# Performance work log

Measured on AMD Instinct MI355X. Metric: run time of the kernel, lower is better.

## Reference

```python
import jax, jax.numpy as jnp
import numpy as np

R_CUT = 5.0
N_NODES = 50000
N_EDGES = 400000
N_GRAPHS = 2500
D = 128        # embedding_size (hardcoded by torch.split(..., 128))
N_RBF = 20
N_BLOCKS = 3
PI = 3.141592653589793


def setup_inputs() -> dict:
    key = jax.random.key(0)
    ks = jax.random.split(key, 32)
    w = lambda k, s: (jax.random.normal(k, s) * 0.05).astype(jnp.float32)
    z = jax.random.randint(ks[0], (N_NODES,), 0, 100)
    edges = jax.random.randint(ks[1], (N_EDGES, 2), 0, N_NODES)
    r_ij = jax.random.uniform(ks[2], (N_EDGES, 1), minval=0.8, maxval=R_CUT, dtype=jnp.float32)
    d = jax.random.normal(ks[3], (N_EDGES, 3), dtype=jnp.float32)
    r_ij_normalized = d / jnp.linalg.norm(d, axis=1, keepdims=True)
    graph_idx = jax.random.randint(ks[4], (N_NODES,), 0, N_GRAPHS)
    return {
        "z": z, "edges": edges, "r_ij": r_ij,
        "r_ij_normalized": r_ij_normalized, "graph_idx": graph_idx,
        "emb": w(ks[5], (100, D)),
        # message blocks (stacked over N_BLOCKS)
        "msg_w1": w(ks[6], (N_BLOCKS, D, D)),   "msg_b1": w(ks[7], (N_BLOCKS, D)),
        "msg_w2": w(ks[8], (N_BLOCKS, D, 3 * D)), "msg_b2": w(ks[9], (N_BLOCKS, 3 * D)),
        "rbf_w": w(ks[10], (N_BLOCKS, N_RBF, 3 * D)), "rbf_b": w(ks[11], (N_BLOCKS, 3 * D)),
        # update blocks
        "upd_U": w(ks[12], (N_BLOCKS, D, D)), "upd_V": w(ks[13], (N_BLOCKS, D, D)),
        "upd_w1": w(ks[14], (N_BLOCKS, 2 * D, D)), "upd_b1": w(ks[15], (N_BLOCKS, D)),
        "upd_w2": w(ks[16], (N_BLOCKS, D, 3 * D)), "upd_b2": w(ks[17], (N_BLOCKS, 3 * D)),
        # readout
        "blue_w1": w(ks[18], (D, D)), "blue_b1": w(ks[19], (D,)),
        "blue_w2": w(ks[20], (D, 1)), "blue_b2": w(ks[21], (1,)),
    }


def _rbf(r, r_cut):
    n = jnp.arange(1, N_RBF + 1, dtype=r.dtype)  # [20]
    return jnp.sin(n * PI / r_cut * r) / r        # [E,20]


def _fcut(r, r_cut):
    return jnp.where(r <= r_cut, 0.5 * (jnp.cos(PI * r / r_cut) + 1.0), 0.0)


def painn_forward(z, edges, r_ij, r_ij_normalized, graph_idx, emb,
                  msg_w1, msg_b1, msg_w2, msg_b2, rbf_w, rbf_b,
                  upd_U, upd_V, upd_w1, upd_b1, upd_w2, upd_b2,
                  blue_w1, blue_b1, blue_w2, blue_b2):
    silu = jax.nn.silu
    src = edges[:, 1]  # gathered (neighbor j)
    dst = edges[:, 0]  # scattered (center i)
    s = emb[z]                                           # [N,128]
    v = jnp.zeros((s.shape[0], 3, D), dtype=r_ij.dtype)  # [N,3,128]
    rbf = _rbf(r_ij, R_CUT)                              # [E,20]
    f_c = _fcut(r_ij, R_CUT)                             # [E,1]
    for i in range(N_BLOCKS):
        # --- message block ---
        rbf_fcut = (rbf @ rbf_w[i] + rbf_b[i]) * f_c            # [E,384]
        s_pass = silu(s @ msg_w1[i] + msg_b1[i]) @ msg_w2[i] + msg_b2[i]  # [N,384]
        pass_out = rbf_fcut * s_pass[src]                        # [E,384]
        d_v, d_s, d_rep = jnp.split(pass_out, 3, axis=-1)        # each [E,128]
        delta_v = v[src] * d_v[:, None, :] + r_ij_normalized[:, :, None] * d_rep[:, None, :]
        s = s + jax.ops.segment_sum(d_s, dst, num_segments=N_NODES)
        v = v + jax.ops.segment_sum(delta_v, dst, num_segments=N_NODES)
        # --- update block ---
        U_v = jnp.einsum('nde,ef->ndf', v, upd_U[i])             # [N,3,128]
        V_v = jnp.einsum('nde,ef->ndf', v, upd_V[i])
        V_norm = jnp.linalg.norm(V_v, axis=1)                    # [N,128]
        sv = jnp.concatenate([V_norm, s], axis=1)                # [N,256]
        a = silu(sv @ upd_w1[i] + upd_b1[i]) @ upd_w2[i] + upd_b2[i]  # [N,384]
        avv, asv, ass = jnp.split(a, 3, axis=1)
        s = s + jnp.sum(U_v * V_v, axis=1) * asv + ass
        v = v + avv[:, None, :] * U_v
    blue = silu(s @ blue_w1 + blue_b1) @ blue_w2 + blue_b2       # [N,1]
    return jax.ops.segment_sum(blue, graph_idx, num_segments=N_GRAPHS)  # [G,1]


def reference(z, edges, r_ij, r_ij_normalized, graph_idx, emb,
              msg_w1, msg_b1, msg_w2, msg_b2, rbf_w, rbf_b,
              upd_U, upd_V, upd_w1, upd_b1, upd_w2, upd_b2,
              blue_w1, blue_b1, blue_w2, blue_b2):
    return painn_forward(z, edges, r_ij, r_ij_normalized, graph_idx, emb,
                         msg_w1, msg_b1, msg_w2, msg_b2, rbf_w, rbf_b,
                         upd_U, upd_V, upd_w1, upd_b1, upd_w2, upd_b2,
                         blue_w1, blue_b1, blue_w2, blue_b2)
```

## Files before the change

kernel.cpp:

```cpp
#include <hip/hip_runtime.h>
#include <hip/hip_bf16.h>
#include <math.h>

#define N_NODES 50000
#define N_EDGES 400000
#define N_GRAPHS 2500
#define D 128
#define D3 384
#define N_RBF 20
#define R_CUT 5.0f
#define PI_F 3.14159265358979f
#define NCH 98
#define GEB 16
#define GLDS_STRIDE 388

typedef __attribute__((ext_vector_type(8))) short bf16x8;
typedef __attribute__((ext_vector_type(4))) float f32x4;

__device__ __forceinline__ float silu_f(float x) {
    return x / (1.0f + __expf(-x));
}
__device__ __forceinline__ short f2bf(float x) {
    union { float f; unsigned u; } v; v.f = x;
    unsigned r = (v.u + 0x7FFFu + ((v.u >> 16) & 1u)) >> 16;
    return (short)r;
}
__device__ __forceinline__ float bf2f(short x) {
    union { unsigned u; float f; } v; v.u = ((unsigned)(unsigned short)x) << 16;
    return v.f;
}

#define MAXJOBS 19
struct PackJobs {
    const float* W[MAXJOBS];
    short* P[MAXJOBS];
    int K[MAXJOBS];
    int N[MAXJOBS];
    int boff[MAXJOBS + 1];
    int njobs;
};
__global__ void k_packall(PackJobs jobs) {
    int b = blockIdx.x;
    int j = 0;
    while (j + 1 < jobs.njobs && b >= jobs.boff[j + 1]) ++j;
    int t = (b - jobs.boff[j]) * 256 + threadIdx.x;
    int K = jobs.K[j], N = jobs.N[j];
    int NKT = K / 32;
    int total = (N / 16) * NKT * 64;
    if (t >= total) return;
    const float* W = jobs.W[j];
    short* P = jobs.P[j];
    int lane = t & 63;
    int kt = (t >> 6) % NKT;
    int nt = (t >> 6) / NKT;
    int k0 = kt * 32 + (lane >> 4) * 8;
    int col = nt * 16 + (lane & 15);
    #pragma unroll
    for (int q = 0; q < 8; ++q)
        P[(size_t)t * 8 + q] = f2bf(W[(size_t)(k0 + q) * N + col]);
}

__global__ void k_packrbf(const float* __restrict__ rbf_w, const float* __restrict__ rbf_b,
                          short* __restrict__ P) {
    int t = blockIdx.x * 256 + threadIdx.x;
    if (t >= 3 * 1536) return;
    int i = t / 1536;
    int r = t - i * 1536;
    int lane = r & 63;
    int nt = r >> 6;
    int col = nt * 16 + (lane & 15);
    int k0 = (lane >> 4) * 8;
    const float* W = rbf_w + (size_t)i * N_RBF * D3;
    const float* B = rbf_b + (size_t)i * D3;
    short* out = P + (size_t)i * 12288 + (size_t)r * 8;
    #pragma unroll
    for (int q = 0; q < 8; ++q) {
        int k = k0 + q;
        float v = (k < N_RBF) ? W[(size_t)k * D3 + col] : ((k == N_RBF) ? B[col] : 0.0f);
        out[q] = f2bf(v);
    }
}

template<int K, int N, bool SILU, int AMODE>
__global__ __launch_bounds__(256) void k_gemm(const void* __restrict__ Aptr,
                                              const void* __restrict__ A2ptr,
                                              const short* __restrict__ Bp,
                                              const float* __restrict__ bias,
                                              short* __restrict__ Cbf, int M) {
    constexpr int NKT = K / 32, NNT = N / 16;
    int lane = threadIdx.x & 63, wv = threadIdx.x >> 6;
    int tile = blockIdx.x * 4 + wv;
    int base = tile * 32;
    if (base >= M) return;
    bool has2 = (base + 16 < M);
    int r16 = lane & 15;
    int kgrp = (lane >> 4) * 8;
    int arow0 = base + r16;
    int arow1 = has2 ? (base + 16 + r16) : arow0;

    bf16x8 a0[NKT], a1[NKT];
    #pragma unroll
    for (int ss = 0; ss < 2; ++ss) {
        int arow = ss ? arow1 : arow0;
        bf16x8* a = ss ? a1 : a0;
        if (AMODE == 0) {
            const short* A = (const short*)Aptr + (size_t)arow * K + kgrp;
            #pragma unroll
            for (int kt = 0; kt < NKT; ++kt) a[kt] = *(const bf16x8*)(A + kt * 32);
        } else if (AMODE == 1) {
            const float* A = (const float*)Aptr + (size_t)arow * K + kgrp;
            #pragma unroll
            for (int kt = 0; kt < NKT; ++kt)
                #pragma unroll
                for (int j = 0; j < 8; ++j) a[kt][j] = f2bf(A[kt * 32 + j]);
        } else {
            const short* A1 = (const short*)Aptr + (size_t)arow * 128 + kgrp;
            const float* A2 = (const float*)A2ptr + (size_t)arow * 128 + kgrp;
            #pragma unroll
            for (int kt = 0; kt < 4 && kt < NKT; ++kt) a[kt] = *(const bf16x8*)(A1 + kt * 32);
            #pragma unroll
            for (int kt = 4; kt < NKT; ++kt)
                #pragma unroll
                for (int j = 0; j < 8; ++j) a[kt][j] = f2bf(A2[(kt - 4) * 32 + j]);
        }
    }

    int crow0 = base + (lane >> 4) * 4;
    int ccol = lane & 15;
    const bf16x8* Bv = (const bf16x8*)Bp;
    #pragma unroll
    for (int nt = 0; nt < NNT; ++nt) {
        f32x4 acc0 = {0.f, 0.f, 0.f, 0.f};
        f32x4 acc1 = {0.f, 0.f, 0.f, 0.f};
        #pragma unroll
        for (int kt = 0; kt < NKT; ++kt) {
            bf16x8 b = Bv[(nt * NKT + kt) * 64 + lane];
            acc0 = __builtin_amdgcn_mfma_f32_16x16x32_bf16(a0[kt], b, acc0, 0, 0, 0);
            acc1 = __builtin_amdgcn_mfma_f32_16x16x32_bf16(a1[kt], b, acc1, 0, 0, 0);
        }
        int col = nt * 16 + ccol;
        float bs = bias ? bias[col] : 0.0f;
        #pragma unroll
        for (int j = 0; j < 4; ++j) {
            float v = acc0[j] + bs;
            if (SILU) v = silu_f(v);
            Cbf[(size_t)(crow0 + j) * N + col] = f2bf(v);
        }
        if (has2) {
            #pragma unroll
            for (int j = 0; j < 4; ++j) {
                float v = acc1[j] + bs;
                if (SILU) v = silu_f(v);
                Cbf[(size_t)(crow0 + 16 + j) * N + col] = f2bf(v);
            }
        }
    }
}

__global__ __launch_bounds__(256) void k_gemmUV(const short* __restrict__ A,
                                                const short* __restrict__ Bp,
                                                short* __restrict__ Cu,
                                                short* __restrict__ Cv, int M) {
    int lane = threadIdx.x & 63, wv = threadIdx.x >> 6;
    int tile = blockIdx.x * 4 + wv;
    int base = tile * 32;
    if (base >= M) return;
    bool has2 = (base + 16 < M);
    int r16 = lane & 15;
    int kgrp = (lane >> 4) * 8;
    const short* Ar0 = A + (size_t)(base + r16) * 128 + kgrp;
    const short* Ar1 = A + (size_t)((has2 ? base + 16 : base) + r16) * 128 + kgrp;
    bf16x8 a0[4], a1[4];
    #pragma unroll
    for (int kt = 0; kt < 4; ++kt) {
        a0[kt] = *(const bf16x8*)(Ar0 + kt * 32);
        a1[kt] = *(const bf16x8*)(Ar1 + kt * 32);
    }
    int crow0 = base + (lane >> 4) * 4;
    int ccol = lane & 15;
    const bf16x8* Bv = (const bf16x8*)Bp;
    #pragma unroll
    for (int nt = 0; nt < 16; ++nt) {
        f32x4 acc0 = {0.f, 0.f, 0.f, 0.f};
        f32x4 acc1 = {0.f, 0.f, 0.f, 0.f};
        #pragma unroll
        for (int kt = 0; kt < 4; ++kt) {
            bf16x8 b = Bv[(nt * 4 + kt) * 64 + lane];
            acc0 = __builtin_amdgcn_mfma_f32_16x16x32_bf16(a0[kt], b, acc0, 0, 0, 0);
            acc1 = __builtin_amdgcn_mfma_f32_16x16x32_bf16(a1[kt], b, acc1, 0, 0, 0);
        }
        int col = nt * 16 + ccol;
        short* C = (col < 128) ? Cu : Cv;
        int cc = col & 127;
        #pragma unroll
        for (int j = 0; j < 4; ++j)
            C[(size_t)(crow0 + j) * 128 + cc] = f2bf(acc0[j]);
        if (has2) {
            #pragma unroll
            for (int j = 0; j < 4; ++j)
                C[(size_t)(crow0 + 16 + j) * 128 + cc] = f2bf(acc1[j]);
        }
    }
}

__global__ void k_embed(const int* __restrict__ z, const float* __restrict__ emb,
                        float* __restrict__ s) {
    int i = blockIdx.x * blockDim.x + threadIdx.x;
    if (i < N_NODES * D) {
        int n = i >> 7, c = i & 127;
        s[i] = emb[z[n] * D + c];
    }
}

__global__ void k_hist(const int* __restrict__ edges, int* __restrict__ cnt) {
    int e = blockIdx.x * 256 + threadIdx.x;
    if (e < N_EDGES) atomicAdd(&cnt[edges[2 * e]], 1);
}

__global__ void k_scan1(const int* __restrict__ cnt, int* __restrict__ csum) {
    int t = threadIdx.x;
    int g = blockIdx.x * 512 + t;
    int v = (g < N_NODES) ? cnt[g] : 0;
    #pragma unroll
    for (int off = 32; off > 0; off >>= 1) v += __shfl_down(v, off, 64);
    __shared__ int ws[8];
    if ((t & 63) == 0) ws[t >> 6] = v;
    __syncthreads();
    if (t == 0) {
        int sum = 0;
        #pragma unroll
        for (int i = 0; i < 8; ++i) sum += ws[i];
        csum[blockIdx.x] = sum;
    }
}

__global__ void k_scan2(const int* __restrict__ csum, int* __restrict__ cbase) {
    if (threadIdx.x == 0 && blockIdx.x == 0) {
        int s = 0;
        for (int i = 0; i < NCH; ++i) { cbase[i] = s; s += csum[i]; }
    }
}

__global__ void k_scan3(const int* __restrict__ cnt, const int* __restrict__ cbase,
                        int* __restrict__ rowptr) {
    __shared__ int buf[512];
    int t = threadIdx.x;
    int g = blockIdx.x * 512 + t;
    int orig = (g < N_NODES) ? cnt[g] : 0;
    buf[t] = orig;
    __syncthreads();
    for (int off = 1; off < 512; off <<= 1) {
        int v = (t >= off) ? buf[t - off] : 0;
        __syncthreads();
        buf[t] += v;
        __syncthreads();
    }
    if (g < N_NODES) rowptr[g] = cbase[blockIdx.x] + buf[t] - orig;
    if (g == 0 && blockIdx.x == 0) rowptr[N_NODES] = N_EDGES;
}

__global__ void k_scatter(const int* __restrict__ edges, const float* __restrict__ r_ij,
                          const float* __restrict__ rhat, const int* __restrict__ rowptr,
                          int* __restrict__ cursor, int* __restrict__ esrc,
                          short* __restrict__ erbf, float4* __restrict__ erhat) {
    int e = blockIdx.x * 256 + threadIdx.x;
    if (e >= N_EDGES) return;
    int dst = edges[2 * e], src = edges[2 * e + 1];
    int p = rowptr[dst] + atomicAdd(&cursor[dst], 1);
    esrc[p] = src;
    float r = r_ij[e];
    float fc = (r <= R_CUT) ? 0.5f * (cosf(PI_F * r / R_CUT) + 1.0f) : 0.0f;
    float inv_r = 1.0f / r;
    short rec[32];
    #pragma unroll
    for (int k = 0; k < N_RBF; ++k)
        rec[k] = f2bf(sinf((float)(k + 1) * (PI_F / R_CUT) * r) * inv_r * fc);
    rec[20] = f2bf(fc);
    #pragma unroll
    for (int k = 21; k < 32; ++k) rec[k] = 0;
    short* out = erbf + (size_t)p * 32;
    #pragma unroll
    for (int k = 0; k < 32; ++k) out[k] = rec[k];
    float4 rh;
    rh.x = rhat[3 * e]; rh.y = rhat[3 * e + 1]; rh.z = rhat[3 * e + 2]; rh.w = 0.f;
    erhat[p] = rh;
}

template<bool HASV>
__global__ __launch_bounds__(128, 4) void k_edge3(
    const int* __restrict__ rowptr, const int* __restrict__ esrc,
    const short* __restrict__ erbf, const float4* __restrict__ erhat,
    const short* __restrict__ pRbf,
    const short* __restrict__ spass, const short* __restrict__ vold,
    float* __restrict__ s, short* __restrict__ vnew) {
    __shared__ short gate_lds[GEB * GLDS_STRIDE];
    __shared__ int   src_lds[GEB];
    __shared__ float4 rh_lds[GEB];
    int tid = threadIdx.x;
    int lane = tid & 63;
    int wv = tid >> 6;
    int c = tid;
    int ntb = wv * 12;
    bf16x8 bfr[12];
    #pragma unroll
    for (int t = 0; t < 12; ++t)
        bfr[t] = *(const bf16x8*)(pRbf + ((size_t)((ntb + t) * 64 + lane)) * 8);
    int r0 = (lane >> 4) * 4;
    int fcol = lane & 15;
    for (int n = blockIdx.x; n < N_NODES; n += gridDim.x) {
        int p0 = rowptr[n], p1 = rowptr[n + 1];
        float sa = 0.f, va0 = 0.f, va1 = 0.f, va2 = 0.f;
        for (int pb = p0; pb < p1; pb += GEB) {
            int erow = pb + (lane & 15);
            if (erow >= p1) erow = p1 - 1;
            bf16x8 afrag = *(const bf16x8*)(erbf + (size_t)erow * 32 + (lane >> 4) * 8);
            if (tid < GEB) {
                int p = pb + tid;
                if (p < p1) { src_lds[tid] = esrc[p]; rh_lds[tid] = erhat[p]; }
            }
            #pragma unroll
            for (int t = 0; t < 12; ++t) {
                f32x4 acc = {0.f, 0.f, 0.f, 0.f};
                acc = __builtin_amdgcn_mfma_f32_16x16x32_bf16(afrag, bfr[t], acc, 0, 0, 0);
                int col = (ntb + t) * 16 + fcol;
                #pragma unroll
                for (int j = 0; j < 4; ++j)
                    gate_lds[(r0 + j) * GLDS_STRIDE + col] = f2bf(acc[j]);
            }
            __syncthreads();
            int pe = (pb + GEB < p1) ? pb + GEB : p1;
            for (int p = pb; p < pe; ++p) {
                int src = src_lds[p - pb];
                float4 rh = rh_lds[p - pb];
                const short* g = gate_lds + (p - pb) * GLDS_STRIDE;
                float a1 = bf2f(g[128 + c]);
                float a2 = bf2f(g[256 + c]);
                const short* sp = spass + (size_t)src * D3;
                float ds = a1 * bf2f(sp[128 + c]);
                float dr = a2 * bf2f(sp[256 + c]);
                sa += ds;
                if (HASV) {
                    float a0 = bf2f(g[c]);
                    float dv = a0 * bf2f(sp[c]);
                    const short* vs = vold + (size_t)src * D3;
                    va0 += bf2f(vs[c]) * dv + rh.x * dr;
                    va1 += bf2f(vs[128 + c]) * dv + rh.y * dr;
                    va2 += bf2f(vs[256 + c]) * dv + rh.z * dr;
                } else {
                    va0 += rh.x * dr;
                    va1 += rh.y * dr;
                    va2 += rh.z * dr;
                }
            }
            __syncthreads();
        }
        s[(size_t)n * D + c] += sa;
        size_t vb = (size_t)n * D3;
        if (HASV) {
            vnew[vb + c]       = f2bf(bf2f(vold[vb + c]) + va0);
            vnew[vb + 128 + c] = f2bf(bf2f(vold[vb + 128 + c]) + va1);
            vnew[vb + 256 + c] = f2bf(bf2f(vold[vb + 256 + c]) + va2);
        } else {
            vnew[vb + c]       = f2bf(va0);
            vnew[vb + 128 + c] = f2bf(va1);
            vnew[vb + 256 + c] = f2bf(va2);
        }
    }
}

__global__ void k_svbuild(const short* __restrict__ Vv, short* __restrict__ Vn) {
    int i = blockIdx.x * 256 + threadIdx.x;
    int n = i >> 7, c = i & 127;
    float acc = 0.f;
    #pragma unroll
    for (int d = 0; d < 3; ++d) {
        float v = bf2f(Vv[(size_t)(n * 3 + d) * D + c]);
        acc += v * v;
    }
    Vn[i] = f2bf(sqrtf(acc));
}

__global__ void k_apply(float* __restrict__ s, short* __restrict__ v,
                        const short* __restrict__ Uv, const short* __restrict__ Vv,
                        const short* __restrict__ a_bf) {
    int i = blockIdx.x * 256 + threadIdx.x;
    int n = i >> 7, c = i & 127;
    float avv = bf2f(a_bf[(size_t)n * D3 + c]);
    float asv = bf2f(a_bf[(size_t)n * D3 + 128 + c]);
    float ass = bf2f(a_bf[(size_t)n * D3 + 256 + c]);
    float scal = 0.f;
    float uvr[3];
    #pragma unroll
    for (int d = 0; d < 3; ++d) {
        float u = bf2f(Uv[(size_t)(n * 3 + d) * D + c]);
        float vv = bf2f(Vv[(size_t)(n * 3 + d) * D + c]);
        uvr[d] = u;
        scal += u * vv;
    }
    s[i] += scal * asv + ass;
    #pragma unroll
    for (int d = 0; d < 3; ++d) {
        size_t idx = (size_t)n * D3 + d * 128 + c;
        v[idx] = f2bf(bf2f(v[idx]) + avv * uvr[d]);
    }
}

__global__ void k_blue_dot(const short* __restrict__ h, const int* __restrict__ graph_idx,
                           const float* __restrict__ w2, const float* __restrict__ b2,
                           float* __restrict__ out) {
    __shared__ float red[4];
    int c = threadIdx.x & 127;
    int n = blockIdx.x * 2 + (threadIdx.x >> 7);
    float val = bf2f(h[(size_t)n * D + c]) * w2[c];
    #pragma unroll
    for (int off = 32; off > 0; off >>= 1) val += __shfl_down(val, off, 64);
    if ((threadIdx.x & 63) == 0) red[threadIdx.x >> 6] = val;
    __syncthreads();
    if (threadIdx.x == 0)   atomicAdd(&out[graph_idx[n]], red[0] + red[1] + b2[0]);
    if (threadIdx.x == 128) atomicAdd(&out[graph_idx[n]], red[2] + red[3] + b2[0]);
}

static inline int g32(int M) { int t = (M + 31) / 32; return (t + 3) / 4; }

extern "C" void kernel_launch(void* const* d_in, const int* in_sizes, int n_in,
                              void* d_out, int out_size, void* d_ws, size_t ws_size,
                              hipStream_t stream) {
    const int*   z         = (const int*)d_in[0];
    const int*   edges     = (const int*)d_in[1];
    const float* r_ij      = (const float*)d_in[2];
    const float* rhat      = (const float*)d_in[3];
    const int*   graph_idx = (const int*)d_in[4];
    const float* emb       = (const float*)d_in[5];
    const float* msg_w1    = (const float*)d_in[6];
    const float* msg_b1    = (const float*)d_in[7];
    const float* msg_w2    = (const float*)d_in[8];
    const float* msg_b2    = (const float*)d_in[9];
    const float* rbf_w     = (const float*)d_in[10];
    const float* rbf_b     = (const float*)d_in[11];
    const float* upd_U     = (const float*)d_in[12];
    const float* upd_V     = (const float*)d_in[13];
    const float* upd_w1    = (const float*)d_in[14];
    const float* upd_b1    = (const float*)d_in[15];
    const float* upd_w2    = (const float*)d_in[16];
    const float* upd_b2    = (const float*)d_in[17];
    const float* blue_w1   = (const float*)d_in[18];
    const float* blue_b1   = (const float*)d_in[19];
    const float* blue_w2   = (const float*)d_in[20];
    const float* blue_b2   = (const float*)d_in[21];
    float* out = (float*)d_out;

    char* ws = (char*)d_ws;
    size_t off = 0;
    auto alloc = [&](size_t bytes) { void* p = ws + off; off += (bytes + 255) & ~(size_t)255; return p; };

    float* s      = (float*)alloc((size_t)N_NODES * D * 4);
    short* bufV0  = (short*)alloc((size_t)N_NODES * D3 * 2);
    short* bufV1  = (short*)alloc((size_t)N_NODES * D3 * 2);
    short* shrd   = (short*)alloc((size_t)N_NODES * D3 * 2);
    short* hbuf   = (short*)alloc((size_t)N_NODES * D * 2);
    short* Vv     = (short*)alloc((size_t)N_NODES * D3 * 2);
    short* Vn     = shrd;
    int*    esrc   = (int*)alloc((size_t)N_EDGES * 4);
    short*  erbf   = (short*)alloc((size_t)N_EDGES * 32 * 2);
    float4* erhat  = (float4*)alloc((size_t)N_EDGES * 16);
    int*    rowptr = (int*)alloc((size_t)(N_NODES + 1) * 4);
    int*    cnt    = (int*)alloc((size_t)N_NODES * 4);
    int*    csum   = (int*)alloc(NCH * 4);
    int*    cbase  = (int*)alloc(NCH * 4);

    short* pBlue = (short*)alloc(16384 * 2);
    short* pRbfAll = (short*)alloc((size_t)3 * 12288 * 2);
    short* pMsgW1[3]; short* pMsgW2[3]; short* pUV[3]; short* pUpdW1[3]; short* pUpdW2[3];
    for (int i = 0; i < 3; ++i) {
        pMsgW1[i] = (short*)alloc(16384 * 2);
        pMsgW2[i] = (short*)alloc(49152 * 2);
        pUV[i]    = (short*)alloc(32768 * 2);
        pUpdW1[i] = (short*)alloc(32768 * 2);
        pUpdW2[i] = (short*)alloc(49152 * 2);
    }

    PackJobs jobs;
    jobs.njobs = 0;
    int bacc = 0;
    auto addjob = [&](const float* W, short* P, int K, int N) {
        int j = jobs.njobs++;
        jobs.W[j] = W; jobs.P[j] = P; jobs.K[j] = K; jobs.N[j] = N;
        jobs.boff[j] = bacc;
        int total = (N / 16) * (K / 32) * 64;
        bacc += (total + 255) / 256;
        jobs.boff[j + 1] = bacc;
    };
    addjob(blue_w1, pBlue, 128, 128);
    for (int i = 0; i < 3; ++i) {
        addjob(msg_w1 + (size_t)i * D * D,     pMsgW1[i], 128, 128);
        addjob(msg_w2 + (size_t)i * D * D3,    pMsgW2[i], 128, 384);
        addjob(upd_U  + (size_t)i * D * D,     pUV[i],          128, 128);
        addjob(upd_V  + (size_t)i * D * D,     pUV[i] + 16384,  128, 128);
        addjob(upd_w1 + (size_t)i * 2 * D * D, pUpdW1[i], 256, 128);
        addjob(upd_w2 + (size_t)i * D * D3,    pUpdW2[i], 128, 384);
    }
    k_packall<<<bacc, 256, 0, stream>>>(jobs);
    k_packrbf<<<18, 256, 0, stream>>>(rbf_w, rbf_b, pRbfAll);

    hipMemsetAsync(cnt, 0, (size_t)N_NODES * 4, stream);
    k_hist<<<(N_EDGES + 255) / 256, 256, 0, stream>>>(edges, cnt);
    k_scan1<<<NCH, 512, 0, stream>>>(cnt, csum);
    k_scan2<<<1, 64, 0, stream>>>(csum, cbase);
    k_scan3<<<NCH, 512, 0, stream>>>(cnt, cbase, rowptr);
    hipMemsetAsync(cnt, 0, (size_t)N_NODES * 4, stream);
    k_scatter<<<(N_EDGES + 255) / 256, 256, 0, stream>>>(edges, r_ij, rhat, rowptr, cnt,
                                                         esrc, erbf, erhat);

    hipMemsetAsync(d_out, 0, (size_t)out_size * sizeof(float), stream);
    k_embed<<<(N_NODES * D) / 256, 256, 0, stream>>>(z, emb, s);

    const int gN  = g32(N_NODES);
    const int gN3 = g32(N_NODES * 3);

    for (int i = 0; i < 3; ++i) {
        short* vstate = (i & 1) ? bufV1 : bufV0;
        short* vscr   = (i & 1) ? bufV0 : bufV1;
        k_gemm<128, 128, true, 1><<<gN, 256, 0, stream>>>(
            s, nullptr, pMsgW1[i], msg_b1 + (size_t)i * D, hbuf, N_NODES);
        k_gemm<128, 384, false, 0><<<gN, 256, 0, stream>>>(
            hbuf, nullptr, pMsgW2[i], msg_b2 + (size_t)i * D3, shrd, N_NODES);
        if (i == 0)
            k_edge3<false><<<4096, 128, 0, stream>>>(rowptr, esrc, erbf, erhat,
                                                     pRbfAll, shrd, vstate, s, vscr);
        else
            k_edge3<true><<<4096, 128, 0, stream>>>(rowptr, esrc, erbf, erhat,
                                                    pRbfAll + (size_t)i * 12288,
                                                    shrd, vstate, s, vscr);
        k_gemmUV<<<gN3, 256, 0, stream>>>(vscr, pUV[i], vstate, Vv, N_NODES * 3);
        k_svbuild<<<(N_NODES * D) / 256, 256, 0, stream>>>(Vv, Vn);
        k_gemm<256, 128, true, 2><<<gN, 256, 0, stream>>>(
            Vn, s, pUpdW1[i], upd_b1 + (size_t)i * D, hbuf, N_NODES);
        k_gemm<128, 384, false, 0><<<gN, 256, 0, stream>>>(
            hbuf, nullptr, pUpdW2[i], upd_b2 + (size_t)i * D3, shrd, N_NODES);
        k_apply<<<(N_NODES * D) / 256, 256, 0, stream>>>(s, vscr, vstate, Vv, shrd);
    }

    k_gemm<128, 128, true, 1><<<gN, 256, 0, stream>>>(
        s, nullptr, pBlue, blue_b1, hbuf, N_NODES);
    k_blue_dot<<<N_NODES / 2, 256, 0, stream>>>(hbuf, graph_idx, blue_w2, blue_b2, out);
}
```

Before: 1.001 ms.

## Split edge loop across two waves with paired bf16 channel loads

The edge aggregation kernel now has each thread handle two adjacent channels using 32-bit packed bf16 loads, and the two waves take alternating edges instead of both walking every edge. Each wave's partial sums are combined through shared memory, and wave 0 writes the final s and v updates with packed stores. This aims to halve the serial edge loop per wave and widen the gather accesses. In exchange it adds an LDS reduction, two extra barriers per node, and leaves wave 1 idle during the final writes.

```diff
diff --git a/kernel.cpp b/kernel.cpp
--- a/kernel.cpp
+++ b/kernel.cpp
@@ -28,6 +28,15 @@
 __device__ __forceinline__ float bf2f(short x) {
     union { unsigned u; float f; } v; v.u = ((unsigned)(unsigned short)x) << 16;
     return v.f;
+}
+__device__ __forceinline__ float bflo(unsigned u) {
+    union { unsigned x; float f; } v; v.x = u << 16; return v.f;
+}
+__device__ __forceinline__ float bfhi(unsigned u) {
+    union { unsigned x; float f; } v; v.x = u & 0xFFFF0000u; return v.f;
+}
+__device__ __forceinline__ unsigned packbf(float a, float b) {
+    return ((unsigned)(unsigned short)f2bf(a)) | (((unsigned)(unsigned short)f2bf(b)) << 16);
 }
 
 #define MAXJOBS 19
@@ -287,7 +296,7 @@
 }
 
 template<bool HASV>
-__global__ __launch_bounds__(128, 4) void k_edge3(
+__global__ __launch_bounds__(128, 4) void k_edge4(
     const int* __restrict__ rowptr, const int* __restrict__ esrc,
     const short* __restrict__ erbf, const float4* __restrict__ erhat,
     const short* __restrict__ pRbf,
@@ -296,11 +305,12 @@
     __shared__ short gate_lds[GEB * GLDS_STRIDE];
     __shared__ int   src_lds[GEB];
     __shared__ float4 rh_lds[GEB];
+    __shared__ float red[64 * 9];
     int tid = threadIdx.x;
     int lane = tid & 63;
     int wv = tid >> 6;
-    int c = tid;
     int ntb = wv * 12;
+    int c0 = lane * 2;
     bf16x8 bfr[12];
     #pragma unroll
     for (int t = 0; t < 12; ++t)
@@ -309,7 +319,8 @@
     int fcol = lane & 15;
     for (int n = blockIdx.x; n < N_NODES; n += gridDim.x) {
         int p0 = rowptr[n], p1 = rowptr[n + 1];
-        float sa = 0.f, va0 = 0.f, va1 = 0.f, va2 = 0.f;
+        float sa0 = 0.f, sa1 = 0.f;
+        float va00 = 0.f, va01 = 0.f, va10 = 0.f, va11 = 0.f, va20 = 0.f, va21 = 0.f;
         for (int pb = p0; pb < p1; pb += GEB) {
             int erow = pb + (lane & 15);
             if (erow >= p1) erow = p1 - 1;
@@ -329,41 +340,67 @@
             }
             __syncthreads();
             int pe = (pb + GEB < p1) ? pb + GEB : p1;
-            for (int p = pb; p < pe; ++p) {
+            for (int p = pb + wv; p < pe; p += 2) {
                 int src = src_lds[p - pb];
                 float4 rh = rh_lds[p - pb];
                 const short* g = gate_lds + (p - pb) * GLDS_STRIDE;
-                float a1 = bf2f(g[128 + c]);
-                float a2 = bf2f(g[256 + c]);
+                unsigned ga1 = *(const unsigned*)(g + 128 + c0);
+                unsigned ga2 = *(const unsigned*)(g + 256 + c0);
                 const short* sp = spass + (size_t)src * D3;
-                float ds = a1 * bf2f(sp[128 + c]);
-                float dr = a2 * bf2f(sp[256 + c]);
-                sa += ds;
+                unsigned sp1 = *(const unsigned*)(sp + 128 + c0);
+                unsigned sp2 = *(const unsigned*)(sp + 256 + c0);
+                sa0 += bflo(ga1) * bflo(sp1);
+                sa1 += bfhi(ga1) * bfhi(sp1);
+                float drl = bflo(ga2) * bflo(sp2);
+                float drh = bfhi(ga2) * bfhi(sp2);
                 if (HASV) {
-                    float a0 = bf2f(g[c]);
-                    float dv = a0 * bf2f(sp[c]);
+                    unsigned ga0 = *(const unsigned*)(g + c0);
+                    unsigned sp0 = *(const unsigned*)(sp + c0);
+                    float dvl = bflo(ga0) * bflo(sp0);
+                    float dvh = bfhi(ga0) * bfhi(sp0);
                     const short* vs = vold + (size_t)src * D3;
-                    va0 += bf2f(vs[c]) * dv + rh.x * dr;
-                    va1 += bf2f(vs[128 + c]) * dv + rh.y * dr;
-                    va2 += bf2f(vs[256 + c]) * dv + rh.z * dr;
+                    unsigned v0 = *(const unsigned*)(vs + c0);
+                    unsigned v1 = *(const unsigned*)(vs + 128 + c0);
+                    unsigned v2 = *(const unsigned*)(vs + 256 + c0);
+                    va00 += bflo(v0) * dvl + rh.x * drl;
+                    va01 += bfhi(v0) * dvh + rh.x * drh;
+                    va10 += bflo(v1) * dvl + rh.y * drl;
+                    va11 += bfhi(v1) * dvh + rh.y * drh;
+                    va20 += bflo(v2) * dvl + rh.z * drl;
+                    va21 += bfhi(v2) * dvh + rh.z * drh;
                 } else {
-                    va0 += rh.x * dr;
-                    va1 += rh.y * dr;
-                    va2 += rh.z * dr;
+                    va00 += rh.x * drl; va01 += rh.x * drh;
+                    va10 += rh.y * drl; va11 += rh.y * drh;
+                    va20 += rh.z * drl; va21 += rh.z * drh;
                 }
             }
             __syncthreads();
         }
-        s[(size_t)n * D + c] += sa;
-        size_t vb = (size_t)n * D3;
-        if (HASV) {
-            vnew[vb + c]       = f2bf(bf2f(vold[vb + c]) + va0);
-            vnew[vb + 128 + c] = f2bf(bf2f(vold[vb + 128 + c]) + va1);
-            vnew[vb + 256 + c] = f2bf(bf2f(vold[vb + 256 + c]) + va2);
-        } else {
-            vnew[vb + c]       = f2bf(va0);
-            vnew[vb + 128 + c] = f2bf(va1);
-            vnew[vb + 256 + c] = f2bf(va2);
+        float* rl = red + lane * 9;
+        __syncthreads();
+        if (wv == 1) {
+            rl[0] = sa0; rl[1] = sa1;
+            rl[2] = va00; rl[3] = va01; rl[4] = va10; rl[5] = va11; rl[6] = va20; rl[7] = va21;
+        }
+        __syncthreads();
+        if (wv == 0) {
+            sa0 += rl[0]; sa1 += rl[1];
+            va00 += rl[2]; va01 += rl[3]; va10 += rl[4]; va11 += rl[5]; va20 += rl[6]; va21 += rl[7];
+            float2 sv = *(float2*)(s + (size_t)n * D + c0);
+            sv.x += sa0; sv.y += sa1;
+            *(float2*)(s + (size_t)n * D + c0) = sv;
+            size_t vb = (size_t)n * D3;
+            if (HASV) {
+                unsigned o0 = *(const unsigned*)(vold + vb + c0);
+                unsigned o1 = *(const unsigned*)(vold + vb + 128 + c0);
+                unsigned o2 = *(const unsigned*)(vold + vb + 256 + c0);
+                va00 += bflo(o0); va01 += bfhi(o0);
+                va10 += bflo(o1); va11 += bfhi(o1);
+                va20 += bflo(o2); va21 += bfhi(o2);
+            }
+            *(unsigned*)(vnew + vb + c0)       = packbf(va00, va01);
+            *(unsigned*)(vnew + vb + 128 + c0) = packbf(va10, va11);
+            *(unsigned*)(vnew + vb + 256 + c0) = packbf(va20, va21);
         }
     }
 }
@@ -525,10 +562,10 @@
         k_gemm<128, 384, false, 0><<<gN, 256, 0, stream>>>(
             hbuf, nullptr, pMsgW2[i], msg_b2 + (size_t)i * D3, shrd, N_NODES);
         if (i == 0)
-            k_edge3<false><<<4096, 128, 0, stream>>>(rowptr, esrc, erbf, erhat,
+            k_edge4<false><<<4096, 128, 0, stream>>>(rowptr, esrc, erbf, erhat,
                                                      pRbfAll, shrd, vstate, s, vscr);
         else
-            k_edge3<true><<<4096, 128, 0, stream>>>(rowptr, esrc, erbf, erhat,
+            k_edge4<true><<<4096, 128, 0, stream>>>(rowptr, esrc, erbf, erhat,
                                                     pRbfAll + (size_t)i * 12288,
                                                     shrd, vstate, s, vscr);
         k_gemmUV<<<gN3, 256, 0, stream>>>(vscr, pUV[i], vstate, Vv, N_NODES * 3);
```

After: 1.009 ms. About the same (+0.8%).
